# Kernel optimization log

Hardware: AMD Instinct MI355X
Metric: run time of the kernel (lower is better)

The kernel has to match this reference:

```python
import jax, jax.numpy as jnp
import numpy as np

B, L, D = 1, 2048, 1024
H, E = 16, 64        # n_heads, d_head
ROT = E // 2         # rotary half-dim
FF = 4 * D
EPS = 1e-6
NEG = -1e30


def setup_inputs() -> dict:
    key = jax.random.key(0)
    ks = jax.random.split(key, 6)
    x = jax.random.normal(ks[0], (B, L, D), jnp.float32)
    theta = jax.random.uniform(ks[1], (B, H, L, ROT), jnp.float32) * (2.0 * np.pi)
    scale = jax.random.normal(ks[2], (B, D), jnp.float32) * 0.1
    w_in = jax.random.normal(ks[3], (7 * D, D), jnp.float32) * (D ** -0.5)
    w_out = jax.random.normal(ks[4], (D, 5 * D), jnp.float32) * ((5 * D) ** -0.5)
    attn_scale = jnp.full((2, H), 10.0, jnp.float32)
    return {"x": x, "theta": theta, "scale": scale,
            "w_in": w_in, "w_out": w_out, "attn_scale": attn_scale}


def _rope(t, cos, sin):
    # t: [b,h,l,E]; rotary applied to first 2*ROT dims (== E here, so no passthrough)
    t1, t2 = t[..., :ROT], t[..., ROT:2 * ROT]
    return jnp.concatenate([t1 * cos - t2 * sin, t2 * cos + t1 * sin], axis=-1)


def _forward(x, theta, scale, w_in, w_out, attn_scale):
    b, l, d = x.shape
    skip = x
    # AdaRMSNorm (no learned weight): rms-normalize then modulate by (1 + scale)
    xn = x * jax.lax.rsqrt(jnp.mean(x ** 2, axis=-1, keepdims=True) + EPS)
    xn = xn * (1.0 + scale[:, None, :])
    # fused QKV + MLP-up projection (torch Linear: y = x @ W.T)
    proj = jnp.einsum('bld,fd->blf', xn, w_in)       # [b,l,7d]
    qkv, up = proj[..., :3 * d], proj[..., 3 * d:]
    up = jax.nn.gelu(up, approximate=True)           # GELU(tanh)
    # 'b l (t nh e) -> t b nh l e'
    qkv = qkv.reshape(b, l, 3, H, E).transpose(2, 0, 3, 1, 4)
    q, k, v = qkv[0], qkv[1], qkv[2]
    # cosine-sim rescaling: q_h * sqrt(s_h)/||q||, k_h * sqrt(s_h)/||k||
    s = jnp.sqrt(attn_scale[0])[None, :, None, None]
    q = q * (s * jax.lax.rsqrt(jnp.sum(q ** 2, axis=-1, keepdims=True) + EPS))
    k = k * (s * jax.lax.rsqrt(jnp.sum(k ** 2, axis=-1, keepdims=True) + EPS))
    # rotary embedding
    cos, sin = jnp.cos(theta), jnp.sin(theta)
    q, k = _rope(q, cos, sin), _rope(k, cos, sin)
    # causal attention with scale = 1.0 (cosine-sim path)
    scores = jnp.einsum('bhqe,bhke->bhqk', q, k)
    causal = jnp.tril(jnp.ones((l, l), bool))
    scores = jnp.where(causal[None, None], scores, NEG)
    probs = jax.nn.softmax(scores, axis=-1)
    attn = jnp.einsum('bhqk,bhke->bhqe', probs, v)
    attn_out = attn.transpose(0, 2, 1, 3).reshape(b, l, d)  # 'b nh l e -> b l (nh e)'
    h = jnp.concatenate([attn_out, up], axis=-1)            # [b,l,5d]
    return jnp.einsum('blf,df->bld', h, w_out) + skip


def reference(x, theta, scale, w_in, w_out, attn_scale):
    return _forward(x, theta, scale, w_in, w_out, attn_scale)
```

## Files before the change

kernel.cpp:

```cpp
#include <hip/hip_runtime.h>

typedef unsigned short u16;
typedef unsigned int u32;
typedef __attribute__((ext_vector_type(8))) short bf16x8;
typedef __attribute__((ext_vector_type(8))) unsigned short u16x8;
typedef __attribute__((ext_vector_type(4))) float f32x4;
typedef __attribute__((ext_vector_type(16))) float f32x16;

#define L_SEQ 2048
#define DMODEL 1024
#define NHEAD 16
#define EHEAD 64
#define FPROJ 7168
#define FCAT 5120
#define NEGINF -1e30f
#define LOG2E 1.44269504088896f
#define EXP2F(x) __builtin_amdgcn_exp2f(x)

__device__ __forceinline__ u16 f2bf(float f) {
  union { float f; u32 u; } v; v.f = f;
  u32 r = v.u + 0x7FFFu + ((v.u >> 16) & 1u);
  return (u16)(r >> 16);
}
__device__ __forceinline__ float bf2f(u16 h) {
  union { u32 u; float f; } v; v.u = ((u32)h) << 16;
  return v.f;
}
__device__ __forceinline__ float gelu_f(float x) {
  float y = 0.7978845608028654f * (x + 0.044715f * x * x * x);
  float t = __expf(-2.0f * fabsf(y));
  float th = (1.0f - t) / (1.0f + t);
  th = (y < 0.0f) ? -th : th;
  return 0.5f * x * (1.0f + th);
}
__device__ __forceinline__ void gld16(void* lds, const void* g) {
  __builtin_amdgcn_global_load_lds((const __attribute__((address_space(1))) u32*)g,
                                   (__attribute__((address_space(3))) u32*)lds, 16, 0, 0);
}

__global__ __launch_bounds__(256) void prep_kernel(const float* __restrict__ a,
                                                   u16* __restrict__ oa, int na4,
                                                   const float* __restrict__ b,
                                                   u16* __restrict__ ob, int nb4,
                                                   int ncvt,
                                                   const float* __restrict__ x,
                                                   const float* __restrict__ scale,
                                                   u16* __restrict__ xn) {
  if ((int)blockIdx.x < ncvt) {
    int i = blockIdx.x * 256 + threadIdx.x;
    const float* src;
    u16* dst;
    int j;
    if (i < na4) { src = a; dst = oa; j = i; }
    else { j = i - na4; if (j >= nb4) return; src = b; dst = ob; }
    float4 v = ((const float4*)src)[j];
    ((u32*)dst)[2 * j] = (u32)f2bf(v.x) | ((u32)f2bf(v.y) << 16);
    ((u32*)dst)[2 * j + 1] = (u32)f2bf(v.z) | ((u32)f2bf(v.w) << 16);
    return;
  }
  int row = blockIdx.x - ncvt;
  const float4 v = ((const float4*)(x + (size_t)row * DMODEL))[threadIdx.x];
  float ss = v.x * v.x + v.y * v.y + v.z * v.z + v.w * v.w;
#pragma unroll
  for (int m = 1; m < 64; m <<= 1) ss += __shfl_xor(ss, m);
  __shared__ float ws[4];
  if ((threadIdx.x & 63) == 0) ws[threadIdx.x >> 6] = ss;
  __syncthreads();
  float tot = ws[0] + ws[1] + ws[2] + ws[3];
  float r = rsqrtf(tot * (1.0f / DMODEL) + 1e-6f);
  float4 sc = ((const float4*)scale)[threadIdx.x];
  u32 w0 = (u32)f2bf(v.x * r * (1.0f + sc.x)) | ((u32)f2bf(v.y * r * (1.0f + sc.y)) << 16);
  u32 w1 = (u32)f2bf(v.z * r * (1.0f + sc.z)) | ((u32)f2bf(v.w * r * (1.0f + sc.w)) << 16);
  u32* dst = (u32*)(xn + (size_t)row * DMODEL);
  dst[2 * threadIdx.x] = w0;
  dst[2 * threadIdx.x + 1] = w1;
}

__device__ __forceinline__ void stage_half(u16* lds, const u16* g, int K, int tid) {
#pragma unroll
  for (int i = 0; i < 2; ++i) {
    int idx = tid + i * 512;
    int r = idx >> 3;
    int gcb = ((idx & 7) << 4) ^ ((r & 7) << 4);
    gld16((char*)lds + idx * 16, (const char*)g + (size_t)r * K * 2 + gcb);
  }
}

#define GFENCE asm volatile("" ::: "memory")
#define VMW0 asm volatile("s_waitcnt vmcnt(0)" ::: "memory")
#define VMW2 asm volatile("s_waitcnt vmcnt(2)" ::: "memory")
#define VMW4 asm volatile("s_waitcnt vmcnt(4)" ::: "memory")
#define VMW6 asm volatile("s_waitcnt vmcnt(6)" ::: "memory")
#define ST_A(BUF, T, HALF) stage_half(sA + (BUF) * 16384 + (HALF) * 8192, \
    Ab + (size_t)((HALF) * 128) * K + (T) * 64, K, tid)
#define ST_B(BUF, T, HALF) stage_half(sB + (BUF) * 16384 + (HALF) * 8192, \
    Bb + (size_t)((HALF) * 128) * K + (T) * 64, K, tid)

#define PHASE(HM, KH, BUFB, WCODE, STCODE) do { \
    __builtin_amdgcn_s_barrier(); \
    const char* ab_ = (const char*)sA + (BUFB) * 32768 + (HM) * 16384 + frow * 128 + ((KH) ? co1 : co0); \
    const char* bb_ = (const char*)sB + (BUFB) * 32768 + (wn * 32 + frow) * 128 + ((KH) ? co1 : co0); \
    bf16x8 af_[8], bv_[2]; \
    _Pragma("unroll") \
    for (int mr = 0; mr < 8; ++mr) af_[mr] = *(const bf16x8*)(ab_ + mr * 2048); \
    bv_[0] = *(const bf16x8*)(bb_); \
    bv_[1] = *(const bf16x8*)(bb_ + 2048); \
    GFENCE; \
    STCODE; \
    WCODE; \
    __builtin_amdgcn_s_setprio(1); \
    _Pragma("unroll") \
    for (int mr = 0; mr < 8; ++mr) { \
      acc[(HM) * 8 + mr][0] = __builtin_amdgcn_mfma_f32_16x16x32_bf16(af_[mr], bv_[0], acc[(HM) * 8 + mr][0], 0, 0, 0); \
      acc[(HM) * 8 + mr][1] = __builtin_amdgcn_mfma_f32_16x16x32_bf16(af_[mr], bv_[1], acc[(HM) * 8 + mr][1], 0, 0, 0); \
    } \
    __builtin_amdgcn_s_setprio(0); \
  } while (0)

template <int OUTMODE>
__global__ __launch_bounds__(512, 2) void gemm256(const u16* __restrict__ A,
                                                  const u16* __restrict__ B,
                                                  u16* __restrict__ C0,
                                                  u16* __restrict__ C1,
                                                  int M, int N, int K) {
  __shared__ __align__(16) u16 smem[65536];
  u16* const sA = smem;
  u16* const sB = smem + 32768;
  const int tid = threadIdx.x;
  const int lane = tid & 63;
  const int wn = tid >> 6;
  const int frow = lane & 15;
  const int kbyte = ((lane >> 4) & 3) << 4;
  const int sw = (frow & 7) << 4;
  const int co0 = kbyte ^ sw;
  const int co1 = (64 | kbyte) ^ sw;

  const int nbx = N >> 8;
  const int nbm = (int)gridDim.x / nbx;
  const int v = (blockIdx.x & 7) * ((int)gridDim.x >> 3) + ((int)blockIdx.x >> 3);
  const int bm = v % nbm, bn = v / nbm;
  const int kper = K / (int)gridDim.y;
  const int kbeg = blockIdx.y * kper;
  const u16* Ab = A + (size_t)(bm * 256) * K + kbeg;
  const u16* Bb = B + (size_t)(bn * 256) * K + kbeg;

  f32x4 acc[16][2] = {};

  const int NT = kper >> 6;
  ST_A(0, 0, 0); ST_B(0, 0, 0); ST_B(0, 0, 1); ST_A(0, 0, 1); ST_A(1, 1, 0);
  VMW2;

  for (int kt = 0; kt < NT; kt += 2) {
    const int t1 = kt + 1;
    const int t2 = (kt + 2 >= NT) ? kt + 2 - NT : kt + 2;
    const int t3 = (kt + 3 >= NT) ? kt + 3 - NT : kt + 3;
    PHASE(0, 0, 0, , ST_B(1, t1, 0));
    PHASE(0, 1, 0, VMW6, ST_B(1, t1, 1));
    PHASE(1, 0, 0, , ST_A(1, t1, 1));
    PHASE(1, 1, 0, VMW4, ST_A(0, t2, 0));
    PHASE(0, 0, 1, , ST_B(0, t2, 0));
    PHASE(0, 1, 1, VMW6, ST_B(0, t2, 1));
    PHASE(1, 0, 1, , ST_A(0, t2, 1));
    PHASE(1, 1, 1, VMW4, ST_A(1, t3, 0));
  }

  VMW0;
  __syncthreads();

  const bool up = (OUTMODE == 1) && (bn >= 12);
  u16* const Cp2 = (OUTMODE == 2) ? C0 + (size_t)blockIdx.y * M * N : nullptr;

#pragma unroll
  for (int hm = 0; hm < 2; ++hm) {
#pragma unroll
    for (int m8 = 0; m8 < 8; ++m8) {
#pragma unroll
      for (int nr = 0; nr < 2; ++nr) {
        int col = wn * 32 + nr * 16 + frow;
#pragma unroll
        for (int r = 0; r < 4; ++r) {
          float vv = acc[hm * 8 + m8][nr][r];
          smem[(m8 * 16 + ((lane >> 4) * 4) + r) * 272 + col] = f2bf(up ? gelu_f(vv) : vv);
        }
      }
    }
    __syncthreads();
#pragma unroll
    for (int j = 0; j < 8; ++j) {
      int row = j * 16 + (tid >> 5);
      int c16 = (tid & 31) * 8;
      u16x8 vv = *(const u16x8*)&smem[row * 272 + c16];
      int gr = bm * 256 + hm * 128 + row;
      int gc = bn * 256 + c16;
      if (OUTMODE == 1) {
        if (!up) *(u16x8*)(C0 + (size_t)gr * (3 * DMODEL) + gc) = vv;
        else     *(u16x8*)(C1 + (size_t)gr * FCAT + (gc - 2048)) = vv;
      } else {
        *(u16x8*)(Cp2 + (size_t)gr * N + gc) = vv;
      }
    }
    __syncthreads();
  }
}

__global__ __launch_bounds__(256) void combine8(const u16* __restrict__ part,
                                                const float* __restrict__ x,
                                                float* __restrict__ out) {
  size_t i = (size_t)(blockIdx.x * 256 + threadIdx.x) * 8;
  float4 x0 = *(const float4*)(x + i);
  float4 x1 = *(const float4*)(x + i + 4);
  float s[8] = {x0.x, x0.y, x0.z, x0.w, x1.x, x1.y, x1.z, x1.w};
#pragma unroll
  for (int p = 0; p < 8; ++p) {
    u16x8 v = *(const u16x8*)(part + (size_t)p * (L_SEQ * DMODEL) + i);
#pragma unroll
    for (int j = 0; j < 8; ++j) s[j] += bf2f(v[j]);
  }
  float4 o0 = {s[0], s[1], s[2], s[3]};
  float4 o1 = {s[4], s[5], s[6], s[7]};
  *(float4*)(out + i) = o0;
  *(float4*)(out + i + 4) = o1;
}

__global__ __launch_bounds__(256) void qkv_prep(const u16* __restrict__ proj,
                                                const float* __restrict__ theta,
                                                const float* __restrict__ attn_scale,
                                                u16* __restrict__ qb, u16* __restrict__ kb,
                                                u16* __restrict__ vb) {
  const int l = blockIdx.x * 4 + (threadIdx.x >> 6);
  const int hd = blockIdx.y;
  const int e = threadIdx.x & 63;
  const u16* pr = proj + (size_t)l * (3 * DMODEL) + hd * EHEAD + e;
  float q = bf2f(pr[0]);
  float k = bf2f(pr[DMODEL]);
  float v = bf2f(pr[2 * DMODEL]);
  float sq = q * q, sk = k * k;
#pragma unroll
  for (int m = 1; m < 64; m <<= 1) {
    sq += __shfl_xor(sq, m);
    sk += __shfl_xor(sk, m);
  }
  float s = sqrtf(attn_scale[hd]);
  q *= LOG2E * s * rsqrtf(sq + 1e-6f);
  k *= s * rsqrtf(sk + 1e-6f);
  float ang = theta[((size_t)hd * L_SEQ + l) * 32 + (e & 31)];
  float cs = __cosf(ang), sn = __sinf(ang);
  float qp = __shfl_xor(q, 32), kp = __shfl_xor(k, 32);
  float qr = (e < 32) ? (q * cs - qp * sn) : (q * cs + qp * sn);
  float kr = (e < 32) ? (k * cs - kp * sn) : (k * cs + kp * sn);
  size_t o = ((size_t)hd * L_SEQ + l) * EHEAD + e;
  qb[o] = f2bf(qr);
  kb[o] = f2bf(kr);
  vb[o] = f2bf(v);
}

__global__ __launch_bounds__(128, 4) void attn_kernel(const u16* __restrict__ qb,
                                                      const u16* __restrict__ kb,
                                                      const u16* __restrict__ vb,
                                                      u16* __restrict__ po,
                                                      float* __restrict__ pm,
                                                      float* __restrict__ pl) {
  const int bid = blockIdx.x;
  const int s = 31 - (bid >> 6);
  const int hd = (bid >> 2) & 15;
  const int c = bid & 3;
  const int tid = threadIdx.x;
  const int lane = tid & 63;
  const int w = tid >> 6;
  const int h = lane >> 5;
  const int ql = lane & 31;
  const int qg = s * 64 + w * 32 + ql;
  const int nt = s + 1;
  const int t0 = (c * nt) >> 2;
  const int t1 = ((c + 1) * nt) >> 2;

  __shared__ u16 sK[64 * 64];
  __shared__ u16 sVT[64 * 64];

  const u16* Kh = kb + (size_t)hd * L_SEQ * EHEAD;
  const u16* Vh = vb + (size_t)hd * L_SEQ * EHEAD;
  const u16* Qh = qb + (size_t)hd * L_SEQ * EHEAD;

  bf16x8 qf[4];
#pragma unroll
  for (int es = 0; es < 4; ++es)
    qf[es] = *(const bf16x8*)(Qh + (size_t)qg * EHEAD + es * 16 + h * 8);

  f32x16 oa[2] = {};
  float m = NEGINF, lsum = 0.0f;

  const int vk = (tid & 15) * 4;
  const int ve = (tid >> 4) * 8;

  for (int kt = t0; kt < t1; ++kt) {
    const int k0 = kt * 64;
    __syncthreads();
#pragma unroll
    for (int i = 0; i < 4; ++i) {
      int r = w * 32 + i * 8 + (lane >> 3);
      const u16* src = Kh + (size_t)(k0 + r) * EHEAD + (((lane & 7) ^ (r & 7)) << 3);
      gld16(sK + (w * 32 + i * 8) * 64 + lane * 8, src);
    }
    u16x8 vr[4];
#pragma unroll
    for (int j = 0; j < 4; ++j)
      vr[j] = *(const u16x8*)(Vh + (size_t)(k0 + vk + j) * EHEAD + ve);
#pragma unroll
    for (int e = 0; e < 8; ++e) {
      int row = ve + e;
      int boff = row * 128 + ((((vk >> 3) ^ (row & 7)) << 4) | ((vk & 4) << 1));
      ushort4 pv;
      pv.x = vr[0][e]; pv.y = vr[1][e]; pv.z = vr[2][e]; pv.w = vr[3][e];
      *(ushort4*)((char*)sVT + boff) = pv;
    }
    __syncthreads();

    f32x16 st[2];
#pragma unroll
    for (int t = 0; t < 2; ++t) {
      f32x16 a = {};
      __builtin_amdgcn_s_setprio(1);
#pragma unroll
      for (int es = 0; es < 4; ++es) {
        int row = t * 32 + ql;
        int boff = row * 128 + (((es * 2 + h) ^ (row & 7)) << 4);
        bf16x8 kf = *(const bf16x8*)((const char*)sK + boff);
        a = __builtin_amdgcn_mfma_f32_32x32x16_bf16(kf, qf[es], a, 0, 0, 0);
      }
      __builtin_amdgcn_s_setprio(0);
      st[t] = a;
    }

    float p[2][16];
    float mx = NEGINF;
    const bool edge = (kt == s);
#pragma unroll
    for (int t = 0; t < 2; ++t)
#pragma unroll
      for (int r = 0; r < 16; ++r) {
        float v = st[t][r];
        if (edge) {
          int kg = k0 + t * 32 + (r & 3) + ((r >> 2) << 3) + h * 4;
          v = (kg > qg) ? NEGINF : v;
        }
        p[t][r] = v;
        mx = fmaxf(mx, v);
      }
    mx = fmaxf(mx, __shfl_xor(mx, 32));
    if (!__all(mx - m <= 8.0f)) {
      float mnew = fmaxf(m, mx);
      float alpha = EXP2F(m - mnew);
      lsum *= alpha;
#pragma unroll
      for (int et = 0; et < 2; ++et)
#pragma unroll
        for (int r = 0; r < 16; ++r) oa[et][r] *= alpha;
      m = mnew;
    }
    float ps = 0.0f;
#pragma unroll
    for (int t = 0; t < 2; ++t)
#pragma unroll
      for (int r = 0; r < 16; ++r) {
        float e_ = EXP2F(p[t][r] - m);
        p[t][r] = e_;
        ps += e_;
      }
    ps += __shfl_xor(ps, 32);
    lsum += ps;

    u32 pk_[2][8];
#pragma unroll
    for (int t = 0; t < 2; ++t)
#pragma unroll
      for (int i = 0; i < 8; ++i)
        asm("v_cvt_pk_bf16_f32 %0, %1, %2" : "=v"(pk_[t][i]) : "v"(p[t][2 * i]), "v"(p[t][2 * i + 1]));

#pragma unroll
    for (int ks = 0; ks < 4; ++ks) {
      const int tp = ks >> 1, base = (ks & 1) * 4;
      u32 s0 = h ? pk_[tp][base + 0] : pk_[tp][base + 2];
      u32 s1 = h ? pk_[tp][base + 1] : pk_[tp][base + 3];
      u32 r0 = (u32)__shfl_xor((int)s0, 32);
      u32 r1 = (u32)__shfl_xor((int)s1, 32);
      union { u32 u[4]; bf16x8 v; } pf;
      pf.u[0] = h ? r0 : pk_[tp][base + 0];
      pf.u[1] = h ? r1 : pk_[tp][base + 1];
      pf.u[2] = h ? pk_[tp][base + 2] : r0;
      pf.u[3] = h ? pk_[tp][base + 3] : r1;
      __builtin_amdgcn_s_setprio(1);
#pragma unroll
      for (int et = 0; et < 2; ++et) {
        int row = et * 32 + ql;
        int boff = row * 128 + (((ks * 2 + h) ^ (row & 7)) << 4);
        bf16x8 vf = *(const bf16x8*)((const char*)sVT + boff);
        oa[et] = __builtin_amdgcn_mfma_f32_32x32x16_bf16(vf, pf.v, oa[et], 0, 0, 0);
      }
      __builtin_amdgcn_s_setprio(0);
    }
  }

  const size_t pidx = (size_t)(s * 16 + hd) * 4 + c;
  u16* orow = po + pidx * 4096 + (size_t)(w * 32 + ql) * 64;
#pragma unroll
  for (int et = 0; et < 2; ++et)
#pragma unroll
    for (int g = 0; g < 4; ++g) {
      ushort4 ov;
      ov.x = f2bf(oa[et][4 * g + 0]);
      ov.y = f2bf(oa[et][4 * g + 1]);
      ov.z = f2bf(oa[et][4 * g + 2]);
      ov.w = f2bf(oa[et][4 * g + 3]);
      *(ushort4*)(orow + et * 32 + g * 8 + h * 4) = ov;
    }
  if (h == 0) {
    pm[pidx * 64 + w * 32 + ql] = m;
    pl[pidx * 64 + w * 32 + ql] = lsum;
  }
}

__global__ __launch_bounds__(256) void attn_merge(const u16* __restrict__ po,
                                                  const float* __restrict__ pm,
                                                  const float* __restrict__ pl,
                                                  u16* __restrict__ hb) {
  const int sh = blockIdx.x;
  const int s = sh >> 4, hd = sh & 15;
  const int r = threadIdx.x >> 2;
  const int ec = (threadIdx.x & 3) << 4;
  float mc[4], wgt[4];
  float M = NEGINF;
#pragma unroll
  for (int c = 0; c < 4; ++c) {
    mc[c] = pm[(size_t)(sh * 4 + c) * 64 + r];
    M = fmaxf(M, mc[c]);
  }
  float L = 0.0f;
#pragma unroll
  for (int c = 0; c < 4; ++c) {
    wgt[c] = EXP2F(mc[c] - M);
    L += pl[(size_t)(sh * 4 + c) * 64 + r] * wgt[c];
  }
  float inv = 1.0f / L;
  float o[16] = {};
#pragma unroll
  for (int c = 0; c < 4; ++c) {
    const u16* pp = po + (size_t)(sh * 4 + c) * 4096 + r * 64 + ec;
    u16x8 v0 = *(const u16x8*)pp;
    u16x8 v1 = *(const u16x8*)(pp + 8);
#pragma unroll
    for (int j = 0; j < 8; ++j) {
      o[j] += wgt[c] * bf2f(v0[j]);
      o[8 + j] += wgt[c] * bf2f(v1[j]);
    }
  }
  u16* dst = hb + (size_t)(s * 64 + r) * FCAT + hd * EHEAD + ec;
  u16x8 out0, out1;
#pragma unroll
  for (int j = 0; j < 8; ++j) {
    out0[j] = f2bf(o[j] * inv);
    out1[j] = f2bf(o[8 + j] * inv);
  }
  *(u16x8*)dst = out0;
  *(u16x8*)(dst + 8) = out1;
}

extern "C" void kernel_launch(void* const* d_in, const int* in_sizes, int n_in,
                              void* d_out, int out_size, void* d_ws, size_t ws_size,
                              hipStream_t stream) {
  const float* x = (const float*)d_in[0];
  const float* theta = (const float*)d_in[1];
  const float* scale = (const float*)d_in[2];
  const float* w_in = (const float*)d_in[3];
  const float* w_out = (const float*)d_in[4];
  const float* attn_scale = (const float*)d_in[5];
  float* out = (float*)d_out;

  char* ws = (char*)d_ws;
  u16* w_out_b = (u16*)ws;   ws += (size_t)DMODEL * FCAT * 2;
  u16* hb = (u16*)ws;        ws += (size_t)L_SEQ * FCAT * 2;
  u16* xn = (u16*)ws;        ws += (size_t)L_SEQ * DMODEL * 2;
  u16* w_in_b = (u16*)ws;    ws += (size_t)FPROJ * DMODEL * 2;
  u16* proj = (u16*)ws;      ws += (size_t)L_SEQ * 3 * DMODEL * 2;
  u16* qb = (u16*)ws;        ws += (size_t)NHEAD * L_SEQ * EHEAD * 2;
  u16* kb = (u16*)ws;        ws += (size_t)NHEAD * L_SEQ * EHEAD * 2;
  u16* vb = (u16*)ws;        ws += (size_t)NHEAD * L_SEQ * EHEAD * 2;
  u16* po = xn;
  float* pm = (float*)(po + (size_t)512 * 4 * 4096);
  float* pl = pm + 512 * 4 * 64;
  u16* part = xn;

  const int na4 = FPROJ * DMODEL / 4, nb4 = DMODEL * FCAT / 4;
  const int ncvt = (na4 + nb4 + 255) / 256;
  prep_kernel<<<ncvt + L_SEQ, 256, 0, stream>>>(w_in, w_in_b, na4, w_out, w_out_b, nb4,
                                                ncvt, x, scale, xn);
  gemm256<1><<<(L_SEQ / 256) * (FPROJ / 256), 512, 0, stream>>>(xn, w_in_b, proj, hb,
                                                                L_SEQ, FPROJ, DMODEL);
  qkv_prep<<<dim3(L_SEQ / 4, NHEAD), 256, 0, stream>>>(proj, theta, attn_scale, qb, kb, vb);
  attn_kernel<<<2048, 128, 0, stream>>>(qb, kb, vb, po, pm, pl);
  attn_merge<<<512, 256, 0, stream>>>(po, pm, pl, hb);
  gemm256<2><<<dim3((L_SEQ / 256) * (DMODEL / 256), 8), 512, 0, stream>>>(hb, w_out_b, part,
                                                                          nullptr, L_SEQ, DMODEL, FCAT);
  combine8<<<L_SEQ * DMODEL / 8 / 256, 256, 0, stream>>>(part, x, out);
}
```

Baseline: 133.6 us.

## Retile GEMM waves to 2x4 grid of 128x64 and simplify K pipeline

Changes each wave's output tile from 256x32 (one column strip of the 256x256 block) to 128x64 (a 2x4 wave grid). This halves the LDS fragment reads per MFMA, since each A and B fragment is now reused across more MFMAs. The finely staggered eight-phase pipeline with partial vmcnt waits is replaced by one phase per 64-wide K tile. Each phase issues the whole next tile's global-to-LDS copies up front and ends with a full vmcnt(0) wait. The simpler schedule may expose more memory latency and adds register pressure from 4 B fragments per wave.

New measurement: 142.3 us. 6.5% more time.

```diff
diff --git a/kernel.cpp b/kernel.cpp
--- a/kernel.cpp
+++ b/kernel.cpp
@@ -88,33 +88,35 @@
 
 #define GFENCE asm volatile("" ::: "memory")
 #define VMW0 asm volatile("s_waitcnt vmcnt(0)" ::: "memory")
-#define VMW2 asm volatile("s_waitcnt vmcnt(2)" ::: "memory")
-#define VMW4 asm volatile("s_waitcnt vmcnt(4)" ::: "memory")
-#define VMW6 asm volatile("s_waitcnt vmcnt(6)" ::: "memory")
 #define ST_A(BUF, T, HALF) stage_half(sA + (BUF) * 16384 + (HALF) * 8192, \
     Ab + (size_t)((HALF) * 128) * K + (T) * 64, K, tid)
 #define ST_B(BUF, T, HALF) stage_half(sB + (BUF) * 16384 + (HALF) * 8192, \
     Bb + (size_t)((HALF) * 128) * K + (T) * 64, K, tid)
 
-#define PHASE(HM, KH, BUFB, WCODE, STCODE) do { \
-    __builtin_amdgcn_s_barrier(); \
-    const char* ab_ = (const char*)sA + (BUFB) * 32768 + (HM) * 16384 + frow * 128 + ((KH) ? co1 : co0); \
-    const char* bb_ = (const char*)sB + (BUFB) * 32768 + (wn * 32 + frow) * 128 + ((KH) ? co1 : co0); \
-    bf16x8 af_[8], bv_[2]; \
+#define MFMA32(CO) do { \
     _Pragma("unroll") \
-    for (int mr = 0; mr < 8; ++mr) af_[mr] = *(const bf16x8*)(ab_ + mr * 2048); \
-    bv_[0] = *(const bf16x8*)(bb_); \
-    bv_[1] = *(const bf16x8*)(bb_ + 2048); \
+    for (int mr = 0; mr < 8; ++mr) af_[mr] = *(const bf16x8*)(abA + mr * 2048 + (CO)); \
+    _Pragma("unroll") \
+    for (int nr = 0; nr < 4; ++nr) bv_[nr] = *(const bf16x8*)(bbB + nr * 2048 + (CO)); \
     GFENCE; \
-    STCODE; \
-    WCODE; \
     __builtin_amdgcn_s_setprio(1); \
     _Pragma("unroll") \
-    for (int mr = 0; mr < 8; ++mr) { \
-      acc[(HM) * 8 + mr][0] = __builtin_amdgcn_mfma_f32_16x16x32_bf16(af_[mr], bv_[0], acc[(HM) * 8 + mr][0], 0, 0, 0); \
-      acc[(HM) * 8 + mr][1] = __builtin_amdgcn_mfma_f32_16x16x32_bf16(af_[mr], bv_[1], acc[(HM) * 8 + mr][1], 0, 0, 0); \
-    } \
+    for (int mr = 0; mr < 8; ++mr) \
+      _Pragma("unroll") \
+      for (int nr = 0; nr < 4; ++nr) \
+        acc[mr][nr] = __builtin_amdgcn_mfma_f32_16x16x32_bf16(af_[mr], bv_[nr], acc[mr][nr], 0, 0, 0); \
     __builtin_amdgcn_s_setprio(0); \
+  } while (0)
+
+#define PHASE1(BUFB, STCODE) do { \
+    __builtin_amdgcn_s_barrier(); \
+    STCODE; \
+    const char* abA = (const char*)sA + (BUFB) * 32768 + wm * 16384 + frow * 128; \
+    const char* bbB = (const char*)sB + (BUFB) * 32768 + (wn2 * 64 + frow) * 128; \
+    bf16x8 af_[8], bv_[4]; \
+    MFMA32(co0); \
+    MFMA32(co1); \
+    VMW0; \
   } while (0)
 
 template <int OUTMODE>
@@ -128,7 +130,9 @@
   u16* const sB = smem + 32768;
   const int tid = threadIdx.x;
   const int lane = tid & 63;
-  const int wn = tid >> 6;
+  const int wv = tid >> 6;
+  const int wm = wv >> 2;
+  const int wn2 = wv & 3;
   const int frow = lane & 15;
   const int kbyte = ((lane >> 4) & 3) << 4;
   const int sw = (frow & 7) << 4;
@@ -144,43 +148,38 @@
   const u16* Ab = A + (size_t)(bm * 256) * K + kbeg;
   const u16* Bb = B + (size_t)(bn * 256) * K + kbeg;
 
-  f32x4 acc[16][2] = {};
+  f32x4 acc[8][4] = {};
 
   const int NT = kper >> 6;
-  ST_A(0, 0, 0); ST_B(0, 0, 0); ST_B(0, 0, 1); ST_A(0, 0, 1); ST_A(1, 1, 0);
-  VMW2;
+  ST_A(0, 0, 0); ST_A(0, 0, 1); ST_B(0, 0, 0); ST_B(0, 0, 1);
+  VMW0;
 
   for (int kt = 0; kt < NT; kt += 2) {
     const int t1 = kt + 1;
-    const int t2 = (kt + 2 >= NT) ? kt + 2 - NT : kt + 2;
-    const int t3 = (kt + 3 >= NT) ? kt + 3 - NT : kt + 3;
-    PHASE(0, 0, 0, , ST_B(1, t1, 0));
-    PHASE(0, 1, 0, VMW6, ST_B(1, t1, 1));
-    PHASE(1, 0, 0, , ST_A(1, t1, 1));
-    PHASE(1, 1, 0, VMW4, ST_A(0, t2, 0));
-    PHASE(0, 0, 1, , ST_B(0, t2, 0));
-    PHASE(0, 1, 1, VMW6, ST_B(0, t2, 1));
-    PHASE(1, 0, 1, , ST_A(0, t2, 1));
-    PHASE(1, 1, 1, VMW4, ST_A(1, t3, 0));
-  }
-
-  VMW0;
+    const int t2 = (kt + 2 >= NT) ? 0 : kt + 2;
+    PHASE1(0, ST_A(1, t1, 0); ST_A(1, t1, 1); ST_B(1, t1, 0); ST_B(1, t1, 1));
+    PHASE1(1, ST_A(0, t2, 0); ST_A(0, t2, 1); ST_B(0, t2, 0); ST_B(0, t2, 1));
+  }
+
   __syncthreads();
 
+  const int lr0 = (lane >> 4) * 4;
   const bool up = (OUTMODE == 1) && (bn >= 12);
   u16* const Cp2 = (OUTMODE == 2) ? C0 + (size_t)blockIdx.y * M * N : nullptr;
 
 #pragma unroll
   for (int hm = 0; hm < 2; ++hm) {
-#pragma unroll
-    for (int m8 = 0; m8 < 8; ++m8) {
-#pragma unroll
-      for (int nr = 0; nr < 2; ++nr) {
-        int col = wn * 32 + nr * 16 + frow;
-#pragma unroll
-        for (int r = 0; r < 4; ++r) {
-          float vv = acc[hm * 8 + m8][nr][r];
-          smem[(m8 * 16 + ((lane >> 4) * 4) + r) * 272 + col] = f2bf(up ? gelu_f(vv) : vv);
+    if (wm == hm) {
+#pragma unroll
+      for (int m8 = 0; m8 < 8; ++m8) {
+#pragma unroll
+        for (int nr = 0; nr < 4; ++nr) {
+          int col = wn2 * 64 + nr * 16 + frow;
+#pragma unroll
+          for (int r = 0; r < 4; ++r) {
+            float vv = acc[m8][nr][r];
+            smem[(m8 * 16 + lr0 + r) * 272 + col] = f2bf(up ? gelu_f(vv) : vv);
+          }
         }
       }
     }
```

## Replace 8-phase pipelined GEMM with simple K=32 double-buffered loop and halve LDS

Applied to the files above, without the earlier changes.

The 256x256 GEMM's eight-phase software pipeline, with 64-wide K tiles, staggered half-tile staging and partial vmcnt waits, is replaced by a plain double-buffered loop over 32-wide K tiles. Each iteration issues the next tile's loads, computes from the current buffer, then waits on all outstanding loads. This halves the LDS footprint to 64 KB, changes the swizzle to fit 64-byte rows, and splits the epilogue into four 64-row chunks to fit the smaller staging area. Intended gains are a smaller LDS footprint and simpler scheduling. The risks are weaker overlap, since every iteration waits on vmcnt(0), and twice as many barriers per unit of K.

Result: slower. 143.1 us (+7.1%).

```diff
diff --git a/kernel.cpp b/kernel.cpp
--- a/kernel.cpp
+++ b/kernel.cpp
@@ -76,46 +76,20 @@
   dst[2 * threadIdx.x + 1] = w1;
 }
 
-__device__ __forceinline__ void stage_half(u16* lds, const u16* g, int K, int tid) {
+__device__ __forceinline__ void stage32(u16* lds, const u16* g, int K, int tid) {
 #pragma unroll
   for (int i = 0; i < 2; ++i) {
     int idx = tid + i * 512;
-    int r = idx >> 3;
-    int gcb = ((idx & 7) << 4) ^ ((r & 7) << 4);
+    int r = idx >> 2, c = idx & 3;
+    int gcb = ((c ^ ((r >> 1) & 3)) << 4);
     gld16((char*)lds + idx * 16, (const char*)g + (size_t)r * K * 2 + gcb);
   }
 }
 
 #define GFENCE asm volatile("" ::: "memory")
 #define VMW0 asm volatile("s_waitcnt vmcnt(0)" ::: "memory")
-#define VMW2 asm volatile("s_waitcnt vmcnt(2)" ::: "memory")
-#define VMW4 asm volatile("s_waitcnt vmcnt(4)" ::: "memory")
-#define VMW6 asm volatile("s_waitcnt vmcnt(6)" ::: "memory")
-#define ST_A(BUF, T, HALF) stage_half(sA + (BUF) * 16384 + (HALF) * 8192, \
-    Ab + (size_t)((HALF) * 128) * K + (T) * 64, K, tid)
-#define ST_B(BUF, T, HALF) stage_half(sB + (BUF) * 16384 + (HALF) * 8192, \
-    Bb + (size_t)((HALF) * 128) * K + (T) * 64, K, tid)
-
-#define PHASE(HM, KH, BUFB, WCODE, STCODE) do { \
-    __builtin_amdgcn_s_barrier(); \
-    const char* ab_ = (const char*)sA + (BUFB) * 32768 + (HM) * 16384 + frow * 128 + ((KH) ? co1 : co0); \
-    const char* bb_ = (const char*)sB + (BUFB) * 32768 + (wn * 32 + frow) * 128 + ((KH) ? co1 : co0); \
-    bf16x8 af_[8], bv_[2]; \
-    _Pragma("unroll") \
-    for (int mr = 0; mr < 8; ++mr) af_[mr] = *(const bf16x8*)(ab_ + mr * 2048); \
-    bv_[0] = *(const bf16x8*)(bb_); \
-    bv_[1] = *(const bf16x8*)(bb_ + 2048); \
-    GFENCE; \
-    STCODE; \
-    WCODE; \
-    __builtin_amdgcn_s_setprio(1); \
-    _Pragma("unroll") \
-    for (int mr = 0; mr < 8; ++mr) { \
-      acc[(HM) * 8 + mr][0] = __builtin_amdgcn_mfma_f32_16x16x32_bf16(af_[mr], bv_[0], acc[(HM) * 8 + mr][0], 0, 0, 0); \
-      acc[(HM) * 8 + mr][1] = __builtin_amdgcn_mfma_f32_16x16x32_bf16(af_[mr], bv_[1], acc[(HM) * 8 + mr][1], 0, 0, 0); \
-    } \
-    __builtin_amdgcn_s_setprio(0); \
-  } while (0)
+#define ST32A(BUF, T) stage32(sA + (BUF) * 8192, Ab + (T) * 32, K, tid)
+#define ST32B(BUF, T) stage32(sB + (BUF) * 8192, Bb + (T) * 32, K, tid)
 
 template <int OUTMODE>
 __global__ __launch_bounds__(512, 2) void gemm256(const u16* __restrict__ A,
@@ -123,17 +97,14 @@
                                                   u16* __restrict__ C0,
                                                   u16* __restrict__ C1,
                                                   int M, int N, int K) {
-  __shared__ __align__(16) u16 smem[65536];
+  __shared__ __align__(16) u16 smem[32768];
   u16* const sA = smem;
-  u16* const sB = smem + 32768;
+  u16* const sB = smem + 16384;
   const int tid = threadIdx.x;
   const int lane = tid & 63;
   const int wn = tid >> 6;
   const int frow = lane & 15;
-  const int kbyte = ((lane >> 4) & 3) << 4;
-  const int sw = (frow & 7) << 4;
-  const int co0 = kbyte ^ sw;
-  const int co1 = (64 | kbyte) ^ sw;
+  const int co = (((lane >> 4) ^ ((frow >> 1) & 3)) << 4);
 
   const int nbx = N >> 8;
   const int nbm = (int)gridDim.x / nbx;
@@ -146,51 +117,71 @@
 
   f32x4 acc[16][2] = {};
 
-  const int NT = kper >> 6;
-  ST_A(0, 0, 0); ST_B(0, 0, 0); ST_B(0, 0, 1); ST_A(0, 0, 1); ST_A(1, 1, 0);
-  VMW2;
-
-  for (int kt = 0; kt < NT; kt += 2) {
-    const int t1 = kt + 1;
-    const int t2 = (kt + 2 >= NT) ? kt + 2 - NT : kt + 2;
-    const int t3 = (kt + 3 >= NT) ? kt + 3 - NT : kt + 3;
-    PHASE(0, 0, 0, , ST_B(1, t1, 0));
-    PHASE(0, 1, 0, VMW6, ST_B(1, t1, 1));
-    PHASE(1, 0, 0, , ST_A(1, t1, 1));
-    PHASE(1, 1, 0, VMW4, ST_A(0, t2, 0));
-    PHASE(0, 0, 1, , ST_B(0, t2, 0));
-    PHASE(0, 1, 1, VMW6, ST_B(0, t2, 1));
-    PHASE(1, 0, 1, , ST_A(0, t2, 1));
-    PHASE(1, 1, 1, VMW4, ST_A(1, t3, 0));
-  }
-
+  const int NT = kper >> 5;
+  ST32A(0, 0); ST32B(0, 0);
   VMW0;
+
+  for (int kt = 0; kt < NT; ++kt) {
+    const int buf = kt & 1;
+    const int tn = (kt + 1 < NT) ? kt + 1 : 0;
+    __builtin_amdgcn_s_barrier();
+    ST32A(buf ^ 1, tn);
+    ST32B(buf ^ 1, tn);
+    const char* ab0 = (const char*)sA + buf * 16384 + frow * 64 + co;
+    const char* bb = (const char*)sB + buf * 16384 + (wn * 32 + frow) * 64 + co;
+    bf16x8 bv0 = *(const bf16x8*)bb;
+    bf16x8 bv1 = *(const bf16x8*)(bb + 1024);
+    bf16x8 af_[8];
+#pragma unroll
+    for (int mr = 0; mr < 8; ++mr) af_[mr] = *(const bf16x8*)(ab0 + mr * 1024);
+    GFENCE;
+    __builtin_amdgcn_s_setprio(1);
+#pragma unroll
+    for (int mr = 0; mr < 8; ++mr) {
+      acc[mr][0] = __builtin_amdgcn_mfma_f32_16x16x32_bf16(af_[mr], bv0, acc[mr][0], 0, 0, 0);
+      acc[mr][1] = __builtin_amdgcn_mfma_f32_16x16x32_bf16(af_[mr], bv1, acc[mr][1], 0, 0, 0);
+    }
+    __builtin_amdgcn_s_setprio(0);
+#pragma unroll
+    for (int mr = 0; mr < 8; ++mr) af_[mr] = *(const bf16x8*)(ab0 + 8192 + mr * 1024);
+    GFENCE;
+    __builtin_amdgcn_s_setprio(1);
+#pragma unroll
+    for (int mr = 0; mr < 8; ++mr) {
+      acc[8 + mr][0] = __builtin_amdgcn_mfma_f32_16x16x32_bf16(af_[mr], bv0, acc[8 + mr][0], 0, 0, 0);
+      acc[8 + mr][1] = __builtin_amdgcn_mfma_f32_16x16x32_bf16(af_[mr], bv1, acc[8 + mr][1], 0, 0, 0);
+    }
+    __builtin_amdgcn_s_setprio(0);
+    VMW0;
+  }
+
   __syncthreads();
 
+  const int lr0 = (lane >> 4) * 4;
   const bool up = (OUTMODE == 1) && (bn >= 12);
   u16* const Cp2 = (OUTMODE == 2) ? C0 + (size_t)blockIdx.y * M * N : nullptr;
 
 #pragma unroll
-  for (int hm = 0; hm < 2; ++hm) {
-#pragma unroll
-    for (int m8 = 0; m8 < 8; ++m8) {
+  for (int q = 0; q < 4; ++q) {
+#pragma unroll
+    for (int m4 = 0; m4 < 4; ++m4) {
 #pragma unroll
       for (int nr = 0; nr < 2; ++nr) {
         int col = wn * 32 + nr * 16 + frow;
 #pragma unroll
         for (int r = 0; r < 4; ++r) {
-          float vv = acc[hm * 8 + m8][nr][r];
-          smem[(m8 * 16 + ((lane >> 4) * 4) + r) * 272 + col] = f2bf(up ? gelu_f(vv) : vv);
+          float vv = acc[q * 4 + m4][nr][r];
+          smem[(m4 * 16 + lr0 + r) * 272 + col] = f2bf(up ? gelu_f(vv) : vv);
         }
       }
     }
     __syncthreads();
 #pragma unroll
-    for (int j = 0; j < 8; ++j) {
-      int row = j * 16 + (tid >> 5);
+    for (int it = 0; it < 4; ++it) {
+      int row = it * 16 + (tid >> 5);
       int c16 = (tid & 31) * 8;
       u16x8 vv = *(const u16x8*)&smem[row * 272 + c16];
-      int gr = bm * 256 + hm * 128 + row;
+      int gr = bm * 256 + q * 64 + row;
       int gc = bn * 256 + c16;
       if (OUTMODE == 1) {
         if (!up) *(u16x8*)(C0 + (size_t)gr * (3 * DMODEL) + gc) = vv;
```
